# Optimization experiments

Hardware: AMD Instinct MI355X
Metric: run time of the kernel (lower is better)

Reference implementation:

```python
import jax, jax.numpy as jnp
import numpy as np

# positions 0,1 = input tensor dims; positions 2,3 = output tensor dims (single entity type)

def _set_partitions(elems):
    if not elems:
        yield []
        return
    first, rest = elems[0], elems[1:]
    for p in _set_partitions(rest):
        for i in range(len(p)):
            yield p[:i] + [p[i] + [first]] + p[i + 1:]
    # note: generator above already covers merging; add singleton case

def _all_set_partitions(elems):
    if not elems:
        return [[]]
    first, rest = elems[0], elems[1:]
    out = []
    for p in _all_set_partitions(rest):
        for i in range(len(p)):
            out.append(p[:i] + [p[i] + [first]] + p[i + 1:])
        out.append([[first]] + p)
    return out

PARTITIONS = _all_set_partitions([0, 1, 2, 3])  # Bell(4) = 15 equivariant partitions


def _apply_partition(X, part, eye, ones):
    """Dense equivalent of diag -> pool -> broadcast -> undiag -> reindex for one partition.
    X: [b, c, n, n]. Returns [b, c, n, n]."""
    pos2blk = {p: bi for bi, blk in enumerate(part) for p in blk}
    blk_letter = {bi: 'defg'[bi] for bi in range(len(part))}
    # step 1: diag (repeated letters) + pool (letters dropped from output)
    in_sub = 'bc' + blk_letter[pos2blk[0]] + blk_letter[pos2blk[1]]
    keep = [bi for bi, blk in enumerate(part)
            if any(p < 2 for p in blk) and any(p >= 2 for p in blk)]
    z_sub = 'bc' + ''.join(blk_letter[bi] for bi in keep)
    Z = jnp.einsum(f'{in_sub}->{z_sub}', X)
    # step 2: broadcast + diag-embed into output positions via eye/ones factors
    out_letter = {2: 'p', 3: 'q'}
    operands, subs = [Z], [z_sub]
    for bi, blk in enumerate(part):
        outpos = [p for p in blk if p >= 2]
        if not outpos:
            continue
        if any(p < 2 for p in blk):  # block tied to a surviving input dim
            for p in outpos:
                operands.append(eye)
                subs.append(blk_letter[bi] + out_letter[p])
        else:  # pure broadcast block
            first = outpos[0]
            operands.append(ones)
            subs.append(out_letter[first])
            for p in outpos[1:]:
                operands.append(eye)
                subs.append(out_letter[first] + out_letter[p])
    return jnp.einsum(','.join(subs) + '->bcpq', *operands)


def setup_inputs() -> dict:
    key = jax.random.key(0)
    k1, k2 = jax.random.split(key)
    B, C_IN, C_OUT, N = 4, 96, 96, 256
    stdv = 0.1 / np.sqrt(C_IN)
    X_in = jax.random.normal(k1, (B, C_IN, N, N), dtype=jnp.float32)
    Y_in = jnp.zeros((B, C_IN, N, N), dtype=jnp.float32)  # only provides output shape
    weights = jax.random.uniform(k2, (15, C_IN, C_OUT), minval=-stdv, maxval=stdv, dtype=jnp.float32)
    bias = jnp.ones((1,), dtype=jnp.float32)
    return {'X_in': X_in, 'Y_in': Y_in, 'weights': weights, 'bias': bias}


def reference(X_in, Y_in, weights, bias):
    n = X_in.shape[-1]
    eye = jnp.eye(n, dtype=X_in.dtype)
    ones = jnp.ones((n,), dtype=X_in.dtype)
    Y = None
    for i, part in enumerate(PARTITIONS):
        Yp = _apply_partition(X_in, part, eye, ones)          # [b, c_in, n, n]
        Yp = jnp.einsum('bcpq,co->bopq', Yp, weights[i])       # channel linear
        Y = Yp if Y is None else Y + Yp
    return Y + bias[0]
```

## Files before the change

### kernel.cpp

```cpp
#include <hip/hip_runtime.h>
#include <hip/hip_bf16.h>

#define NN 256
#define CIN 96
#define COUT 96
#define BB 4
#define NBC (BB * CIN)
#define SEG (NBC * NN)

typedef __attribute__((ext_vector_type(8))) short short8;
typedef __attribute__((ext_vector_type(4))) float f32x4;

__device__ __forceinline__ float waveReduceSum(float v) {
    #pragma unroll
    for (int m = 32; m >= 1; m >>= 1) v += __shfl_xor(v, m, 64);
    return v;
}

__device__ __forceinline__ unsigned int packbf2(float lo, float hi) {
    __hip_bfloat162 h = __float22bfloat162_rn(make_float2(lo, hi));
    unsigned int u;
    __builtin_memcpy(&u, &h, 4);
    return u;
}

__device__ __forceinline__ short8 u4_to_s8(uint4 u) {
    short8 r;
    __builtin_memcpy(&r, &u, 16);
    return r;
}

__global__ __launch_bounds__(256) void k_aux(const float* __restrict__ X,
                                             float* __restrict__ rows,
                                             float* __restrict__ diag,
                                             float* __restrict__ colsP,
                                             float* __restrict__ TSp) {
    const int blk = blockIdx.x;
    const int ch = blk & 3, bc = blk >> 2;
    const float* Xp = X + (size_t)bc * (NN * NN) + (size_t)ch * 64 * NN;
    const int tid = threadIdx.x;
    const int w = tid >> 6, lane = tid & 63;

    __shared__ float colPart[4][NN];
    __shared__ float sred[4];

    float4 csum = make_float4(0.f, 0.f, 0.f, 0.f);
    #pragma unroll
    for (int b2 = 0; b2 < 2; ++b2) {
        float4 v[8];
        #pragma unroll
        for (int j = 0; j < 8; ++j) {
            const int r = w * 16 + b2 * 8 + j;
            v[j] = *(const float4*)(Xp + (size_t)r * NN + lane * 4);
        }
        #pragma unroll
        for (int j = 0; j < 8; ++j) {
            csum.x += v[j].x; csum.y += v[j].y; csum.z += v[j].z; csum.w += v[j].w;
            float rs = waveReduceSum(v[j].x + v[j].y + v[j].z + v[j].w);
            if (lane == 0)
                rows[(size_t)bc * NN + ch * 64 + w * 16 + b2 * 8 + j] = rs;
        }
    }
    *(float4*)&colPart[w][lane * 4] = csum;

    if (w == 0) {
        float dv = Xp[(size_t)lane * NN + ch * 64 + lane];
        diag[(size_t)bc * NN + ch * 64 + lane] = dv;
        float t1 = waveReduceSum(dv);
        if (lane == 0) TSp[(ch * NBC + bc) * 2 + 0] = t1;
    }
    __syncthreads();

    float col = colPart[0][tid] + colPart[1][tid] + colPart[2][tid] + colPart[3][tid];
    colsP[(size_t)ch * SEG + (size_t)bc * NN + tid] = col;
    float s1 = waveReduceSum(col);
    if (lane == 0) sred[w] = s1;
    __syncthreads();
    if (tid == 0)
        TSp[(ch * NBC + bc) * 2 + 1] = sred[0] + sred[1] + sred[2] + sred[3];
}

__global__ __launch_bounds__(1024) void k_pqg(const float* __restrict__ W,
                                              const float* __restrict__ rows,
                                              const float* __restrict__ diag,
                                              const float* __restrict__ colsP,
                                              const float* __restrict__ TSp,
                                              const float* __restrict__ bias,
                                              float* __restrict__ Pw,
                                              float* __restrict__ Qw,
                                              float* __restrict__ Gw) {
    const int bo = blockIdx.x;
    const int b = bo / COUT, o = bo % COUT;
    const int qtr = threadIdx.x >> 8;
    const int p = threadIdx.x & 255;

    __shared__ float red[3][5][256];

    float P = 0.f, Q = 0.f, G = 0.f, s = 0.f, gs = 0.f;
    const int cbeg = qtr * 24, cend = cbeg + 24;
    for (int c = cbeg; c < cend; ++c) {
        const int bcq = b * CIN + c;
        const size_t base = (size_t)bcq * NN;
        float r  = rows[base + p];
        float cl = colsP[0 * SEG + base + p] + colsP[1 * SEG + base + p]
                 + colsP[2 * SEG + base + p] + colsP[3 * SEG + base + p];
        float dg = diag[base + p];
        const float* wp = W + c * COUT + o;
        #define WI(i) wp[(i) * CIN * COUT]
        P += WI(12) * r + WI(7)  * cl + WI(5) * dg;
        Q += WI(13) * r + WI(10) * cl + WI(9) * dg;
        G += WI(3)  * r + WI(1)  * cl + WI(0) * dg;
        float Tv = TSp[(0 * NBC + bcq) * 2] + TSp[(1 * NBC + bcq) * 2]
                 + TSp[(2 * NBC + bcq) * 2] + TSp[(3 * NBC + bcq) * 2];
        float Sv = TSp[(0 * NBC + bcq) * 2 + 1] + TSp[(1 * NBC + bcq) * 2 + 1]
                 + TSp[(2 * NBC + bcq) * 2 + 1] + TSp[(3 * NBC + bcq) * 2 + 1];
        s  += WI(11) * Tv + WI(14) * Sv;
        gs += WI(2)  * Tv + WI(4)  * Sv;
        #undef WI
    }
    if (qtr) {
        red[qtr - 1][0][p] = P; red[qtr - 1][1][p] = Q; red[qtr - 1][2][p] = G;
        red[qtr - 1][3][p] = s; red[qtr - 1][4][p] = gs;
    }
    __syncthreads();
    if (qtr == 0) {
        P += red[0][0][p] + red[1][0][p] + red[2][0][p];
        Q += red[0][1][p] + red[1][1][p] + red[2][1][p];
        G += red[0][2][p] + red[1][2][p] + red[2][2][p];
        s += red[0][3][p] + red[1][3][p] + red[2][3][p];
        gs += red[0][4][p] + red[1][4][p] + red[2][4][p];
        const size_t ob = (size_t)bo * NN;
        Pw[ob + p] = P + s + bias[0];
        Qw[ob + p] = Q;
        Gw[ob + p] = G + gs;
    }
}

#define XPLANE 324
#define WPLANE 100

__global__ __launch_bounds__(512, 1) void k_main(const float* __restrict__ X,
                                                 const float* __restrict__ W,
                                                 const float* __restrict__ Pw,
                                                 const float* __restrict__ Qw,
                                                 const float* __restrict__ Gw,
                                                 float* __restrict__ Y) {
    __shared__ __align__(16) unsigned int XAs[16 * XPLANE];
    __shared__ __align__(16) unsigned int XBs[16 * XPLANE];
    __shared__ __align__(16) unsigned int W8s[16 * WPLANE];
    __shared__ __align__(16) unsigned int W6s[16 * WPLANE];

    const int orig = blockIdx.x + 16 * (blockIdx.y + 16 * blockIdx.z);
    const int work = (orig & 7) * 128 + (orig >> 3);
    const int tq = work & 15, tp = (work >> 4) & 15, b = work >> 8;

    const int tid = threadIdx.x;
    const int w = tid >> 6, lane = tid & 63;
    const int sp = lane >> 2, sq4 = (lane & 3) * 4;
    const int col = lane & 15, g = lane >> 4;

    f32x4 acc[6][2];
    #pragma unroll
    for (int m = 0; m < 6; ++m) {
        acc[m][0] = f32x4{0.f, 0.f, 0.f, 0.f};
        acc[m][1] = f32x4{0.f, 0.f, 0.f, 0.f};
    }

    const float* Xb  = X + (size_t)b * CIN * NN * NN;
    const float* G1  = Xb + (size_t)(tp * 16) * NN + tq * 16;
    const float* G2  = Xb + (size_t)(tq * 16) * NN + tp * 16;
    const float* w8g = W + 8 * CIN * COUT;
    const float* w6g = W + 6 * CIN * COUT;

    for (int c0 = 0; c0 < CIN; c0 += 32) {
        __syncthreads();

        #pragma unroll
        for (int h = 0; h < 2; ++h) {
            const int cw = w + 8 * h;
            const size_t cb = (size_t)(c0 + 2 * cw) * (NN * NN);
            const float* pa = G1 + cb + sp * NN + sq4;
            float4 a0 = *(const float4*)pa;
            float4 a1 = *(const float4*)(pa + NN * NN);
            uint4 pk;
            pk.x = packbf2(a0.x, a1.x);
            pk.y = packbf2(a0.y, a1.y);
            pk.z = packbf2(a0.z, a1.z);
            pk.w = packbf2(a0.w, a1.w);
            *(uint4*)&XAs[cw * XPLANE + sp * 20 + sq4] = pk;

            const float* pb = G2 + cb + sp * NN + sq4;
            float4 b0 = *(const float4*)pb;
            float4 b1 = *(const float4*)(pb + NN * NN);
            unsigned int* dB = &XBs[cw * XPLANE + sp];
            dB[(sq4 + 0) * 20] = packbf2(b0.x, b1.x);
            dB[(sq4 + 1) * 20] = packbf2(b0.y, b1.y);
            dB[(sq4 + 2) * 20] = packbf2(b0.z, b1.z);
            dB[(sq4 + 3) * 20] = packbf2(b0.w, b1.w);
        }
        #pragma unroll
        for (int it = 0; it < 3; ++it) {
            const int i  = tid + it * 512;
            const int cw = i / 96, o = i - cw * 96;
            const int cg = (c0 + 2 * cw) * COUT + o;
            W8s[cw * WPLANE + o] = packbf2(w8g[cg], w8g[cg + COUT]);
            W6s[cw * WPLANE + o] = packbf2(w6g[cg], w6g[cg + COUT]);
        }
        __syncthreads();

        const unsigned int* xab = &XAs[4 * g * XPLANE + w * 20 + col];
        const unsigned int* xbb = &XBs[4 * g * XPLANE + w * 20 + col];
        uint4 u;
        u.x = xab[0]; u.y = xab[XPLANE]; u.z = xab[2 * XPLANE]; u.w = xab[3 * XPLANE];
        short8 xd0 = u4_to_s8(u);
        u.x = xab[160]; u.y = xab[XPLANE + 160]; u.z = xab[2 * XPLANE + 160]; u.w = xab[3 * XPLANE + 160];
        short8 xd1 = u4_to_s8(u);
        u.x = xbb[0]; u.y = xbb[XPLANE]; u.z = xbb[2 * XPLANE]; u.w = xbb[3 * XPLANE];
        short8 xt0 = u4_to_s8(u);
        u.x = xbb[160]; u.y = xbb[XPLANE + 160]; u.z = xbb[2 * XPLANE + 160]; u.w = xbb[3 * XPLANE + 160];
        short8 xt1 = u4_to_s8(u);

        #pragma unroll
        for (int m = 0; m < 6; ++m) {
            const unsigned int* wp8 = &W8s[4 * g * WPLANE + m * 16 + col];
            const unsigned int* wp6 = &W6s[4 * g * WPLANE + m * 16 + col];
            uint4 v8, v6;
            v8.x = wp8[0]; v8.y = wp8[WPLANE]; v8.z = wp8[2 * WPLANE]; v8.w = wp8[3 * WPLANE];
            v6.x = wp6[0]; v6.y = wp6[WPLANE]; v6.z = wp6[2 * WPLANE]; v6.w = wp6[3 * WPLANE];
            short8 w8f = u4_to_s8(v8);
            short8 w6f = u4_to_s8(v6);
            acc[m][0] = __builtin_amdgcn_mfma_f32_16x16x32_bf16(xd0, w8f, acc[m][0], 0, 0, 0);
            acc[m][0] = __builtin_amdgcn_mfma_f32_16x16x32_bf16(xt0, w6f, acc[m][0], 0, 0, 0);
            acc[m][1] = __builtin_amdgcn_mfma_f32_16x16x32_bf16(xd1, w8f, acc[m][1], 0, 0, 0);
            acc[m][1] = __builtin_amdgcn_mfma_f32_16x16x32_bf16(xt1, w6f, acc[m][1], 0, 0, 0);
        }
    }

    const int p0 = tp * 16 + w;
    const int q4 = tq * 16 + g * 4;
    const bool diagblk = (tp == tq);
    #pragma unroll
    for (int m = 0; m < 6; ++m) {
        const int o = m * 16 + col;
        const size_t ob = (size_t)(b * COUT + o) * NN;
        const float4 qf = *(const float4*)&Qw[ob + q4];
        #pragma unroll
        for (int rr = 0; rr < 2; ++rr) {
            const int p = p0 + rr * 8;
            const float pv = Pw[ob + p];
            float4 out;
            out.x = acc[m][rr][0] + pv + qf.x;
            out.y = acc[m][rr][1] + pv + qf.y;
            out.z = acc[m][rr][2] + pv + qf.z;
            out.w = acc[m][rr][3] + pv + qf.w;
            if (diagblk) {
                const float gv = Gw[ob + p];
                const int d = (p & 15) - g * 4;
                if (d == 0) out.x += gv;
                else if (d == 1) out.y += gv;
                else if (d == 2) out.z += gv;
                else if (d == 3) out.w += gv;
            }
            *(float4*)&Y[(ob + p) * NN + q4] = out;
        }
    }
}

extern "C" void kernel_launch(void* const* d_in, const int* in_sizes, int n_in,
                              void* d_out, int out_size, void* d_ws, size_t ws_size,
                              hipStream_t stream) {
    const float* X    = (const float*)d_in[0];
    const float* W    = (const float*)d_in[2];
    const float* bias = (const float*)d_in[3];
    float* Y = (float*)d_out;

    float* ws    = (float*)d_ws;
    float* rows  = ws;
    float* diag  = ws + SEG;
    float* colsP = ws + 2 * (size_t)SEG;
    float* Pw    = ws + 6 * (size_t)SEG;
    float* Qw    = ws + 7 * (size_t)SEG;
    float* Gw    = ws + 8 * (size_t)SEG;
    float* TSp   = ws + 9 * (size_t)SEG;

    k_aux<<<NBC * 4, 256, 0, stream>>>(X, rows, diag, colsP, TSp);
    k_pqg<<<BB * COUT, 1024, 0, stream>>>(W, rows, diag, colsP, TSp, bias, Pw, Qw, Gw);
    k_main<<<dim3(16, 16, BB), 512, 0, stream>>>(X, W, Pw, Qw, Gw, Y);
}
```

Before: 127.8 us.

## Prefetch next X chunk into registers in main loop; pre-reduce column partials

The main MFMA kernel now issues the global loads for the next 32-channel chunk right after the shared-memory barrier, so they overlap with the current chunk's MFMA work (register double-buffering). A new small kernel pre-sums the four column-partial buffers and the T/S partials once, and k_pqg reads the pre-reduced arrays using 512 threads split into two halves instead of 1024 split into four. This avoids recomputing the partial sums 96 times per batch, at the cost of one extra launch, a workspace region, and higher register pressure in k_main.

```diff
diff --git a/kernel.cpp b/kernel.cpp
--- a/kernel.cpp
+++ b/kernel.cpp
@@ -80,55 +80,61 @@
         TSp[(ch * NBC + bc) * 2 + 1] = sred[0] + sred[1] + sred[2] + sred[3];
 }
 
-__global__ __launch_bounds__(1024) void k_pqg(const float* __restrict__ W,
-                                              const float* __restrict__ rows,
-                                              const float* __restrict__ diag,
-                                              const float* __restrict__ colsP,
-                                              const float* __restrict__ TSp,
-                                              const float* __restrict__ bias,
-                                              float* __restrict__ Pw,
-                                              float* __restrict__ Qw,
-                                              float* __restrict__ Gw) {
+__global__ __launch_bounds__(256) void k_sum(const float* __restrict__ colsP,
+                                             const float* __restrict__ TSp,
+                                             float* __restrict__ cols,
+                                             float* __restrict__ TSa) {
+    const int bc = blockIdx.x;
+    const int p = threadIdx.x;
+    const size_t base = (size_t)bc * NN + p;
+    cols[base] = colsP[0 * (size_t)SEG + base] + colsP[1 * (size_t)SEG + base]
+               + colsP[2 * (size_t)SEG + base] + colsP[3 * (size_t)SEG + base];
+    if (p < 2)
+        TSa[bc * 2 + p] = TSp[(0 * NBC + bc) * 2 + p] + TSp[(1 * NBC + bc) * 2 + p]
+                        + TSp[(2 * NBC + bc) * 2 + p] + TSp[(3 * NBC + bc) * 2 + p];
+}
+
+__global__ __launch_bounds__(512) void k_pqg(const float* __restrict__ W,
+                                             const float* __restrict__ rows,
+                                             const float* __restrict__ cols,
+                                             const float* __restrict__ diag,
+                                             const float* __restrict__ TSa,
+                                             const float* __restrict__ bias,
+                                             float* __restrict__ Pw,
+                                             float* __restrict__ Qw,
+                                             float* __restrict__ Gw) {
     const int bo = blockIdx.x;
     const int b = bo / COUT, o = bo % COUT;
-    const int qtr = threadIdx.x >> 8;
+    const int half = threadIdx.x >> 8;
     const int p = threadIdx.x & 255;
 
-    __shared__ float red[3][5][256];
+    __shared__ float red[5][256];
 
     float P = 0.f, Q = 0.f, G = 0.f, s = 0.f, gs = 0.f;
-    const int cbeg = qtr * 24, cend = cbeg + 24;
+    const int cbeg = half * 48, cend = cbeg + 48;
     for (int c = cbeg; c < cend; ++c) {
         const int bcq = b * CIN + c;
         const size_t base = (size_t)bcq * NN;
         float r  = rows[base + p];
-        float cl = colsP[0 * SEG + base + p] + colsP[1 * SEG + base + p]
-                 + colsP[2 * SEG + base + p] + colsP[3 * SEG + base + p];
+        float cl = cols[base + p];
         float dg = diag[base + p];
         const float* wp = W + c * COUT + o;
         #define WI(i) wp[(i) * CIN * COUT]
         P += WI(12) * r + WI(7)  * cl + WI(5) * dg;
         Q += WI(13) * r + WI(10) * cl + WI(9) * dg;
         G += WI(3)  * r + WI(1)  * cl + WI(0) * dg;
-        float Tv = TSp[(0 * NBC + bcq) * 2] + TSp[(1 * NBC + bcq) * 2]
-                 + TSp[(2 * NBC + bcq) * 2] + TSp[(3 * NBC + bcq) * 2];
-        float Sv = TSp[(0 * NBC + bcq) * 2 + 1] + TSp[(1 * NBC + bcq) * 2 + 1]
-                 + TSp[(2 * NBC + bcq) * 2 + 1] + TSp[(3 * NBC + bcq) * 2 + 1];
+        float Tv = TSa[bcq * 2 + 0];
+        float Sv = TSa[bcq * 2 + 1];
         s  += WI(11) * Tv + WI(14) * Sv;
         gs += WI(2)  * Tv + WI(4)  * Sv;
         #undef WI
     }
-    if (qtr) {
-        red[qtr - 1][0][p] = P; red[qtr - 1][1][p] = Q; red[qtr - 1][2][p] = G;
-        red[qtr - 1][3][p] = s; red[qtr - 1][4][p] = gs;
+    if (half == 1) {
+        red[0][p] = P; red[1][p] = Q; red[2][p] = G; red[3][p] = s; red[4][p] = gs;
     }
     __syncthreads();
-    if (qtr == 0) {
-        P += red[0][0][p] + red[1][0][p] + red[2][0][p];
-        Q += red[0][1][p] + red[1][1][p] + red[2][1][p];
-        G += red[0][2][p] + red[1][2][p] + red[2][2][p];
-        s += red[0][3][p] + red[1][3][p] + red[2][3][p];
-        gs += red[0][4][p] + red[1][4][p] + red[2][4][p];
+    if (half == 0) {
+        P += red[0][p]; Q += red[1][p]; G += red[2][p]; s += red[3][p]; gs += red[4][p];
         const size_t ob = (size_t)bo * NN;
         Pw[ob + p] = P + s + bias[0];
         Qw[ob + p] = Q;
@@ -172,31 +178,54 @@
     const float* w8g = W + 8 * CIN * COUT;
     const float* w6g = W + 6 * CIN * COUT;
 
+    const int cw0 = w, cw1 = w + 8;
+
+    float4 a00, a01, b00, b01;
+    float4 a10, a11, b10, b11;
+
+    #define LOADG(C0) { \
+        const size_t cb0 = (size_t)((C0) + 2 * cw0) * (NN * NN); \
+        const size_t cb1 = (size_t)((C0) + 2 * cw1) * (NN * NN); \
+        const float* pa0 = G1 + cb0 + sp * NN + sq4; \
+        a00 = *(const float4*)pa0; \
+        a01 = *(const float4*)(pa0 + NN * NN); \
+        const float* pb0 = G2 + cb0 + sp * NN + sq4; \
+        b00 = *(const float4*)pb0; \
+        b01 = *(const float4*)(pb0 + NN * NN); \
+        const float* pa1 = G1 + cb1 + sp * NN + sq4; \
+        a10 = *(const float4*)pa1; \
+        a11 = *(const float4*)(pa1 + NN * NN); \
+        const float* pb1 = G2 + cb1 + sp * NN + sq4; \
+        b10 = *(const float4*)pb1; \
+        b11 = *(const float4*)(pb1 + NN * NN); }
+
+    LOADG(0);
+
     for (int c0 = 0; c0 < CIN; c0 += 32) {
         __syncthreads();
 
-        #pragma unroll
-        for (int h = 0; h < 2; ++h) {
-            const int cw = w + 8 * h;
-            const size_t cb = (size_t)(c0 + 2 * cw) * (NN * NN);
-            const float* pa = G1 + cb + sp * NN + sq4;
-            float4 a0 = *(const float4*)pa;
-            float4 a1 = *(const float4*)(pa + NN * NN);
+        {
             uint4 pk;
-            pk.x = packbf2(a0.x, a1.x);
-            pk.y = packbf2(a0.y, a1.y);
-            pk.z = packbf2(a0.z, a1.z);
-            pk.w = packbf2(a0.w, a1.w);
-            *(uint4*)&XAs[cw * XPLANE + sp * 20 + sq4] = pk;
-
-            const float* pb = G2 + cb + sp * NN + sq4;
-            float4 b0 = *(const float4*)pb;
-            float4 b1 = *(const float4*)(pb + NN * NN);
-            unsigned int* dB = &XBs[cw * XPLANE + sp];
-            dB[(sq4 + 0) * 20] = packbf2(b0.x, b1.x);
-            dB[(sq4 + 1) * 20] = packbf2(b0.y, b1.y);
-            dB[(sq4 + 2) * 20] = packbf2(b0.z, b1.z);
-            dB[(sq4 + 3) * 20] = packbf2(b0.w, b1.w);
+            pk.x = packbf2(a00.x, a01.x);
+            pk.y = packbf2(a00.y, a01.y);
+            pk.z = packbf2(a00.z, a01.z);
+            pk.w = packbf2(a00.w, a01.w);
+            *(uint4*)&XAs[cw0 * XPLANE + sp * 20 + sq4] = pk;
+            pk.x = packbf2(a10.x, a11.x);
+            pk.y = packbf2(a10.y, a11.y);
+            pk.z = packbf2(a10.z, a11.z);
+            pk.w = packbf2(a10.w, a11.w);
+            *(uint4*)&XAs[cw1 * XPLANE + sp * 20 + sq4] = pk;
+            unsigned int* dB0 = &XBs[cw0 * XPLANE + sp];
+            dB0[(sq4 + 0) * 20] = packbf2(b00.x, b01.x);
+            dB0[(sq4 + 1) * 20] = packbf2(b00.y, b01.y);
+            dB0[(sq4 + 2) * 20] = packbf2(b00.z, b01.z);
+            dB0[(sq4 + 3) * 20] = packbf2(b00.w, b01.w);
+            unsigned int* dB1 = &XBs[cw1 * XPLANE + sp];
+            dB1[(sq4 + 0) * 20] = packbf2(b10.x, b11.x);
+            dB1[(sq4 + 1) * 20] = packbf2(b10.y, b11.y);
+            dB1[(sq4 + 2) * 20] = packbf2(b10.z, b11.z);
+            dB1[(sq4 + 3) * 20] = packbf2(b10.w, b11.w);
         }
         #pragma unroll
         for (int it = 0; it < 3; ++it) {
@@ -207,6 +236,8 @@
             W6s[cw * WPLANE + o] = packbf2(w6g[cg], w6g[cg + COUT]);
         }
         __syncthreads();
+
+        if (c0 + 32 < CIN) LOADG(c0 + 32);
 
         const unsigned int* xab = &XAs[4 * g * XPLANE + w * 20 + col];
         const unsigned int* xbb = &XBs[4 * g * XPLANE + w * 20 + col];
@@ -235,6 +266,7 @@
             acc[m][1] = __builtin_amdgcn_mfma_f32_16x16x32_bf16(xt1, w6f, acc[m][1], 0, 0, 0);
         }
     }
+    #undef LOADG
 
     const int p0 = tp * 16 + w;
     const int q4 = tq * 16 + g * 4;
@@ -276,14 +308,17 @@
 
     float* ws    = (float*)d_ws;
     float* rows  = ws;
-    float* diag  = ws + SEG;
+    float* diag  = ws + (size_t)SEG;
     float* colsP = ws + 2 * (size_t)SEG;
     float* Pw    = ws + 6 * (size_t)SEG;
     float* Qw    = ws + 7 * (size_t)SEG;
     float* Gw    = ws + 8 * (size_t)SEG;
     float* TSp   = ws + 9 * (size_t)SEG;
+    float* TSa   = ws + 9 * (size_t)SEG + 4096;
+    float* cols  = ws + 10 * (size_t)SEG;
 
     k_aux<<<NBC * 4, 256, 0, stream>>>(X, rows, diag, colsP, TSp);
-    k_pqg<<<BB * COUT, 1024, 0, stream>>>(W, rows, diag, colsP, TSp, bias, Pw, Qw, Gw);
+    k_sum<<<NBC, 256, 0, stream>>>(colsP, TSp, cols, TSa);
+    k_pqg<<<BB * COUT, 512, 0, stream>>>(W, rows, cols, diag, TSa, bias, Pw, Qw, Gw);
     k_main<<<dim3(16, 16, BB), 512, 0, stream>>>(X, W, Pw, Qw, Gw, Y);
 }
```

After: 111.4 us. 12.8% less time.
